# Kernel tuning notes

Hardware: AMD Instinct MI355X
Metric: run time of the kernel (lower is better)

The kernel has to match this reference:

```python
import jax, jax.numpy as jnp
import numpy as np

N, E = 50000, 400000
NODE_IN, EDGE_IN, HID = 16, 8, 16


def setup_inputs() -> dict:
    key = jax.random.key(0)
    ks = jax.random.split(key, 20)
    s = 0.05
    inp = {
        "x": jax.random.normal(ks[0], (N, NODE_IN), jnp.float32),
        "edge_attr": jax.random.normal(ks[1], (E, EDGE_IN), jnp.float32),
        # edge_nn1: Linear(edge_in, hid) -> ReLU -> Linear(hid, node_in*hid)
        "e1_w1": jax.random.normal(ks[2], (EDGE_IN, HID), jnp.float32) * s,
        "e1_b1": jnp.zeros((HID,), jnp.float32),
        "e1_w2": jax.random.normal(ks[3], (HID, NODE_IN * HID), jnp.float32) * s,
        "e1_b2": jnp.zeros((NODE_IN * HID,), jnp.float32),
        # NNConv1 root weight + bias
        "root1": jax.random.normal(ks[4], (NODE_IN, HID), jnp.float32) * s,
        "bias1": jnp.zeros((HID,), jnp.float32),
        # edge_nn2: Linear(edge_in, hid) -> ReLU -> Linear(hid, hid*hid)
        "e2_w1": jax.random.normal(ks[5], (EDGE_IN, HID), jnp.float32) * s,
        "e2_b1": jnp.zeros((HID,), jnp.float32),
        "e2_w2": jax.random.normal(ks[6], (HID, HID * HID), jnp.float32) * s,
        "e2_b2": jnp.zeros((HID * HID,), jnp.float32),
        # NNConv2 root weight + bias
        "root2": jax.random.normal(ks[7], (HID, HID), jnp.float32) * s,
        "bias2": jnp.zeros((HID,), jnp.float32),
        # q_head
        "q_w": jax.random.normal(ks[8], (HID, 1), jnp.float32) * s,
        "q_b": jnp.zeros((1,), jnp.float32),
        "edge_index": jax.random.randint(ks[9], (2, E), 0, N, jnp.int64),
    }
    return inp


def _nnconv(x, src, dst, edge_attr, w1, b1, w2, b2, root, bias, in_ch, out_ch, n_nodes):
    # edge MLP -> per-edge weight matrix [E, in_ch, out_ch]
    h = jax.nn.relu(edge_attr @ w1 + b1)
    W = (h @ w2 + b2).reshape(-1, in_ch, out_ch)
    # gather source features, per-edge matmul (bmm)
    msg = jnp.einsum('ei,eio->eo', x[src], W)  # [E, out_ch]
    # scatter-mean into target nodes
    summed = jax.ops.segment_sum(msg, dst, num_segments=n_nodes)
    cnt = jax.ops.segment_sum(jnp.ones((dst.shape[0], 1), x.dtype), dst, num_segments=n_nodes)
    agg = summed / jnp.maximum(cnt, 1.0)
    # root transform + bias (NNConv update)
    return agg + x @ root + bias


def reference(x, edge_attr, e1_w1, e1_b1, e1_w2, e1_b2, root1, bias1,
              e2_w1, e2_b1, e2_w2, e2_b2, root2, bias2, q_w, q_b, edge_index):
    src, dst = edge_index[0], edge_index[1]
    h = jax.nn.relu(_nnconv(x, src, dst, edge_attr, e1_w1, e1_b1, e1_w2, e1_b2,
                            root1, bias1, NODE_IN, HID, N))
    h = jax.nn.relu(_nnconv(h, src, dst, edge_attr, e2_w1, e2_b1, e2_w2, e2_b2,
                            root2, bias2, HID, HID, N))
    return (h @ q_w + q_b).squeeze(-1)  # [N]
```

## Files before the change

kernel.cpp:

```cpp
#include <hip/hip_runtime.h>

#define NN 50000
#define NE 400000
#define SCAN_N (2 * NN)
#define SA_BLOCKS ((SCAN_N + 255) / 256)
#define YSTRIDE 276


__global__ __launch_bounds__(256) void hist2_kernel(
    const int* __restrict__ eidx, int* __restrict__ cnt)
{
    int e = blockIdx.x * 256 + threadIdx.x;
    if (e < NE) {
        atomicAdd(&cnt[eidx[e]], 1);
        atomicAdd(&cnt[NN + eidx[NE + e]], 1);
    }
}

template <int NT>
__device__ __forceinline__ int block_excl_scan(int v, int tid)
{
    __shared__ int wsum[NT / 64];
    int lane = tid & 63, w = tid >> 6;
    int incl = v;
#pragma unroll
    for (int d = 1; d < 64; d <<= 1) {
        int t = __shfl_up(incl, d, 64);
        if (lane >= d) incl += t;
    }
    if (lane == 63) wsum[w] = incl;
    __syncthreads();
    if (tid == 0) {
        int s = 0;
#pragma unroll
        for (int k = 0; k < NT / 64; ++k) { int t = wsum[k]; wsum[k] = s; s += t; }
    }
    __syncthreads();
    return incl - v + wsum[w];
}

__global__ __launch_bounds__(256) void scan_a_kernel(
    const int* __restrict__ cnt, int* __restrict__ bsum)
{
    __shared__ int wsum[4];
    int tid = threadIdx.x;
    int i = blockIdx.x * 256 + tid;
    int v = (i < SCAN_N) ? cnt[i] : 0;
#pragma unroll
    for (int d = 32; d >= 1; d >>= 1) v += __shfl_down(v, d, 64);
    if ((tid & 63) == 0) wsum[tid >> 6] = v;
    __syncthreads();
    if (tid == 0) bsum[blockIdx.x] = wsum[0] + wsum[1] + wsum[2] + wsum[3];
}

__global__ __launch_bounds__(512) void scan_b_kernel(
    int* __restrict__ bsum, int* __restrict__ offs_all)
{
    int tid = threadIdx.x;
    int v = (tid < SA_BLOCKS) ? bsum[tid] : 0;
    int excl = block_excl_scan<512>(v, tid);
    if (tid < SA_BLOCKS) bsum[tid] = excl;
    if (tid == SA_BLOCKS - 1) offs_all[SCAN_N] = excl + v;
}

__global__ __launch_bounds__(256) void scan_c_kernel(
    int* __restrict__ cnt ,
    const int* __restrict__ bsum, int* __restrict__ offs_all)
{
    int tid = threadIdx.x;
    int i = blockIdx.x * 256 + tid;
    int v = (i < SCAN_N) ? cnt[i] : 0;
    int excl = block_excl_scan<256>(v, tid) + bsum[blockIdx.x];
    if (i < SCAN_N) { offs_all[i] = excl; cnt[i] = excl; }
}

__global__ __launch_bounds__(256) void fill2_kernel(
    const int* __restrict__ eidx, int* __restrict__ cursor,
    int2* __restrict__ ordsrc)
{
    int e = blockIdx.x * 256 + threadIdx.x;
    if (e < NE) {
        int s = eidx[e], d = eidx[NE + e];
        int ps = atomicAdd(&cursor[s], 1);
        int pd = atomicAdd(&cursor[NN + d], 1) - NE;
        ordsrc[ps] = make_int2(e, pd);
    }
}

__global__ __launch_bounds__(256) void edge_fused_kernel(
    const float* __restrict__ xin,
    const float* __restrict__ ea,
    const int2*  __restrict__ ordsrc,
    const int*   __restrict__ offs_src,
    const float* __restrict__ w1,
    const float* __restrict__ b1,
    const float* __restrict__ w2,
    const float* __restrict__ b2,
    float* __restrict__ msg)
{
    __shared__ float xl[16 * 16];
    __shared__ float Yl[16 * YSTRIDE];
    __shared__ int so[17];

    int tid = threadIdx.x;
    int n0 = blockIdx.x * 16;

    {
        int node = tid >> 4, i = tid & 15;
        xl[tid] = xin[(size_t)(n0 + node) * 16 + i];
    }
    if (tid < 17) so[tid] = offs_src[n0 + tid];
    __syncthreads();

    int o = tid & 15;
    {
        int k = tid >> 4;
        float w[16];
#pragma unroll
        for (int i = 0; i < 16; ++i) w[i] = w2[k * 256 + i * 16 + o];
#pragma unroll 4
        for (int node = 0; node < 16; ++node) {
            const float4* xr = (const float4*)&xl[node * 16];
            float4 x0 = xr[0], x1 = xr[1], x2 = xr[2], x3 = xr[3];
            float acc = x0.x * w[0] + x0.y * w[1] + x0.z * w[2] + x0.w * w[3]
                      + x1.x * w[4] + x1.y * w[5] + x1.z * w[6] + x1.w * w[7]
                      + x2.x * w[8] + x2.y * w[9] + x2.z * w[10] + x2.w * w[11]
                      + x3.x * w[12] + x3.y * w[13] + x3.z * w[14] + x3.w * w[15];
            Yl[node * YSTRIDE + k * 16 + o] = acc;
        }
    }
    {
        int node = tid >> 4;
        float w[16];
#pragma unroll
        for (int i = 0; i < 16; ++i) w[i] = b2[i * 16 + o];
        const float4* xr = (const float4*)&xl[node * 16];
        float4 x0 = xr[0], x1 = xr[1], x2 = xr[2], x3 = xr[3];
        float acc = x0.x * w[0] + x0.y * w[1] + x0.z * w[2] + x0.w * w[3]
                  + x1.x * w[4] + x1.y * w[5] + x1.z * w[6] + x1.w * w[7]
                  + x2.x * w[8] + x2.y * w[9] + x2.z * w[10] + x2.w * w[11]
                  + x3.x * w[12] + x3.y * w[13] + x3.z * w[14] + x3.w * w[15];
        Yl[node * YSTRIDE + 256 + o] = acc;
    }
    __syncthreads();

    int j0 = so[0], j1 = so[16];
    for (int j = j0 + tid; j < j1; j += 256) {
        int node = 0;
#pragma unroll
        for (int t = 1; t < 16; ++t) node += (j >= so[t]) ? 1 : 0;

        int2 od = ordsrc[j];
        int e = od.x, pd = od.y;

        const float4* av = (const float4*)(ea + (size_t)e * 8);
        float4 a0 = av[0], a1 = av[1];
        float a[8] = {a0.x, a0.y, a0.z, a0.w, a1.x, a1.y, a1.z, a1.w};

        float hid[16];
#pragma unroll
        for (int jj = 0; jj < 16; ++jj) hid[jj] = b1[jj];
#pragma unroll
        for (int c = 0; c < 8; ++c)
#pragma unroll
            for (int jj = 0; jj < 16; ++jj) hid[jj] += a[c] * w1[c * 16 + jj];
#pragma unroll
        for (int jj = 0; jj < 16; ++jj) hid[jj] = fmaxf(hid[jj], 0.0f);

        const float4* Yr = (const float4*)&Yl[node * YSTRIDE];
        float4 m0 = Yr[64], m1 = Yr[65], m2 = Yr[66], m3 = Yr[67];
#pragma unroll
        for (int k = 0; k < 16; ++k) {
            float hk = hid[k];
            float4 y0 = Yr[k * 4 + 0], y1 = Yr[k * 4 + 1];
            float4 y2 = Yr[k * 4 + 2], y3 = Yr[k * 4 + 3];
            m0.x = fmaf(hk, y0.x, m0.x); m0.y = fmaf(hk, y0.y, m0.y);
            m0.z = fmaf(hk, y0.z, m0.z); m0.w = fmaf(hk, y0.w, m0.w);
            m1.x = fmaf(hk, y1.x, m1.x); m1.y = fmaf(hk, y1.y, m1.y);
            m1.z = fmaf(hk, y1.z, m1.z); m1.w = fmaf(hk, y1.w, m1.w);
            m2.x = fmaf(hk, y2.x, m2.x); m2.y = fmaf(hk, y2.y, m2.y);
            m2.z = fmaf(hk, y2.z, m2.z); m2.w = fmaf(hk, y2.w, m2.w);
            m3.x = fmaf(hk, y3.x, m3.x); m3.y = fmaf(hk, y3.y, m3.y);
            m3.z = fmaf(hk, y3.z, m3.z); m3.w = fmaf(hk, y3.w, m3.w);
        }
        float4* mp = (float4*)(msg + (size_t)pd * 16);
        mp[0] = m0; mp[1] = m1; mp[2] = m2; mp[3] = m3;
    }
}

__global__ __launch_bounds__(256) void node1_gather(
    const float* __restrict__ x, const float* __restrict__ msg,
    const int* __restrict__ offs_dst,
    const float* __restrict__ root, const float* __restrict__ bias,
    float* __restrict__ out)
{
    int t = blockIdx.x * 256 + threadIdx.x;
    int n = t >> 4, o = t & 15;
    if (n >= NN) return;

    int j0 = offs_dst[n] - NE, j1 = offs_dst[n + 1] - NE;
    float sum = 0.0f;
    for (int j = j0; j < j1; ++j) sum += msg[(size_t)j * 16 + o];
    float inv = 1.0f / (float)((j1 - j0) > 0 ? (j1 - j0) : 1);
    float acc = sum * inv + bias[o];

    float xo = x[(size_t)n * 16 + o];
#pragma unroll
    for (int i = 0; i < 16; ++i)
        acc += __shfl(xo, i, 16) * root[i * 16 + o];

    out[(size_t)n * 16 + o] = fmaxf(acc, 0.0f);
}

__global__ __launch_bounds__(256) void node2q_gather(
    const float* __restrict__ h1, const float* __restrict__ msg,
    const int* __restrict__ offs_dst,
    const float* __restrict__ root, const float* __restrict__ bias,
    const float* __restrict__ qw, const float* __restrict__ qb,
    float* __restrict__ out)
{
    int t = blockIdx.x * 256 + threadIdx.x;
    int n = t >> 4, o = t & 15;
    if (n >= NN) return;

    int j0 = offs_dst[n] - NE, j1 = offs_dst[n + 1] - NE;
    float sum = 0.0f;
    for (int j = j0; j < j1; ++j) sum += msg[(size_t)j * 16 + o];
    float inv = 1.0f / (float)((j1 - j0) > 0 ? (j1 - j0) : 1);
    float acc = sum * inv + bias[o];

    float xo = h1[(size_t)n * 16 + o];
#pragma unroll
    for (int i = 0; i < 16; ++i)
        acc += __shfl(xo, i, 16) * root[i * 16 + o];

    float q = fmaxf(acc, 0.0f) * qw[o];
#pragma unroll
    for (int d = 8; d >= 1; d >>= 1) q += __shfl_down(q, d, 16);
    if (o == 0) out[n] = q + qb[0];
}

extern "C" void kernel_launch(void* const* d_in, const int* in_sizes, int n_in,
                              void* d_out, int out_size, void* d_ws, size_t ws_size,
                              hipStream_t stream) {
    const float* x     = (const float*)d_in[0];
    const float* ea    = (const float*)d_in[1];
    const float* e1w1  = (const float*)d_in[2];
    const float* e1b1  = (const float*)d_in[3];
    const float* e1w2  = (const float*)d_in[4];
    const float* e1b2  = (const float*)d_in[5];
    const float* root1 = (const float*)d_in[6];
    const float* bias1 = (const float*)d_in[7];
    const float* e2w1  = (const float*)d_in[8];
    const float* e2b1  = (const float*)d_in[9];
    const float* e2w2  = (const float*)d_in[10];
    const float* e2b2  = (const float*)d_in[11];
    const float* root2 = (const float*)d_in[12];
    const float* bias2 = (const float*)d_in[13];
    const float* qw    = (const float*)d_in[14];
    const float* qb    = (const float*)d_in[15];
    const int*   eidx  = (const int*)d_in[16];

    float* msg      = (float*)d_ws;
    float* h1       = msg + (size_t)16 * NE;
    int*   offs_all = (int*)(h1 + (size_t)16 * NN);
    int*   cursor   = offs_all + SCAN_N + 1;
    int2*  ordsrc   = (int2*)(cursor + SCAN_N);
    int*   bsum     = (int*)(ordsrc + NE);

    int eblocks = (NE + 255) / 256;
    int gblocks = NN / 16;
    int nblocks = (NN * 16 + 255) / 256;

    hipMemsetAsync(cursor, 0, (size_t)SCAN_N * sizeof(int), stream);
    hist2_kernel<<<eblocks, 256, 0, stream>>>(eidx, cursor);
    scan_a_kernel<<<SA_BLOCKS, 256, 0, stream>>>(cursor, bsum);
    scan_b_kernel<<<1, 512, 0, stream>>>(bsum, offs_all);
    scan_c_kernel<<<SA_BLOCKS, 256, 0, stream>>>(cursor, bsum, offs_all);
    fill2_kernel<<<eblocks, 256, 0, stream>>>(eidx, cursor, ordsrc);

    edge_fused_kernel<<<gblocks, 256, 0, stream>>>(x, ea, ordsrc, offs_all,
                                                   e1w1, e1b1, e1w2, e1b2, msg);
    node1_gather<<<nblocks, 256, 0, stream>>>(x, msg, offs_all + NN, root1,
                                              bias1, h1);

    edge_fused_kernel<<<gblocks, 256, 0, stream>>>(h1, ea, ordsrc, offs_all,
                                                   e2w1, e2b1, e2w2, e2b2, msg);
    node2q_gather<<<nblocks, 256, 0, stream>>>(h1, msg, offs_all + NN, root2,
                                               bias2, qw, qb, (float*)d_out);
}
```

Before: 256.5 us.

## Replace CSR scan with capped source-group buckets and atomic scatter-add aggregation

Removes the histogram and three-pass scan and the dst-sorted message buffer. Edges are now bucketed per group of 16 source nodes into fixed-capacity slots, and destination counts are gathered in the same pass. The edge kernel accumulates messages straight into per-node sums with float atomics, and the layer-1 node update is fused into the layer-2 edge kernel. This cuts the number of launches and the message-buffer traffic, at the cost of many global atomics. It also relies on no group exceeding CAP edges: extra edges in a group would be silently dropped, and the atomic summation order is nondeterministic.

```diff
diff --git a/kernel.cpp b/kernel.cpp
--- a/kernel.cpp
+++ b/kernel.cpp
@@ -2,135 +2,83 @@
 
 #define NN 50000
 #define NE 400000
-#define SCAN_N (2 * NN)
-#define SA_BLOCKS ((SCAN_N + 255) / 256)
+#define NG (NN / 16)
+#define CAP 320
 #define YSTRIDE 276
 
 
-__global__ __launch_bounds__(256) void hist2_kernel(
-    const int* __restrict__ eidx, int* __restrict__ cnt)
-{
-    int e = blockIdx.x * 256 + threadIdx.x;
-    if (e < NE) {
-        atomicAdd(&cnt[eidx[e]], 1);
-        atomicAdd(&cnt[NN + eidx[NE + e]], 1);
-    }
-}
-
-template <int NT>
-__device__ __forceinline__ int block_excl_scan(int v, int tid)
-{
-    __shared__ int wsum[NT / 64];
-    int lane = tid & 63, w = tid >> 6;
-    int incl = v;
-#pragma unroll
-    for (int d = 1; d < 64; d <<= 1) {
-        int t = __shfl_up(incl, d, 64);
-        if (lane >= d) incl += t;
-    }
-    if (lane == 63) wsum[w] = incl;
-    __syncthreads();
-    if (tid == 0) {
-        int s = 0;
-#pragma unroll
-        for (int k = 0; k < NT / 64; ++k) { int t = wsum[k]; wsum[k] = s; s += t; }
-    }
-    __syncthreads();
-    return incl - v + wsum[w];
-}
-
-__global__ __launch_bounds__(256) void scan_a_kernel(
-    const int* __restrict__ cnt, int* __restrict__ bsum)
-{
-    __shared__ int wsum[4];
-    int tid = threadIdx.x;
-    int i = blockIdx.x * 256 + tid;
-    int v = (i < SCAN_N) ? cnt[i] : 0;
-#pragma unroll
-    for (int d = 32; d >= 1; d >>= 1) v += __shfl_down(v, d, 64);
-    if ((tid & 63) == 0) wsum[tid >> 6] = v;
-    __syncthreads();
-    if (tid == 0) bsum[blockIdx.x] = wsum[0] + wsum[1] + wsum[2] + wsum[3];
-}
-
-__global__ __launch_bounds__(512) void scan_b_kernel(
-    int* __restrict__ bsum, int* __restrict__ offs_all)
-{
-    int tid = threadIdx.x;
-    int v = (tid < SA_BLOCKS) ? bsum[tid] : 0;
-    int excl = block_excl_scan<512>(v, tid);
-    if (tid < SA_BLOCKS) bsum[tid] = excl;
-    if (tid == SA_BLOCKS - 1) offs_all[SCAN_N] = excl + v;
-}
-
-__global__ __launch_bounds__(256) void scan_c_kernel(
-    int* __restrict__ cnt ,
-    const int* __restrict__ bsum, int* __restrict__ offs_all)
-{
-    int tid = threadIdx.x;
-    int i = blockIdx.x * 256 + tid;
-    int v = (i < SCAN_N) ? cnt[i] : 0;
-    int excl = block_excl_scan<256>(v, tid) + bsum[blockIdx.x];
-    if (i < SCAN_N) { offs_all[i] = excl; cnt[i] = excl; }
-}
-
-__global__ __launch_bounds__(256) void fill2_kernel(
+__global__ __launch_bounds__(256) void fill_hist_kernel(
     const int* __restrict__ eidx, int* __restrict__ cursor,
-    int2* __restrict__ ordsrc)
+    int* __restrict__ cnt_dst, int2* __restrict__ ord)
 {
     int e = blockIdx.x * 256 + threadIdx.x;
     if (e < NE) {
         int s = eidx[e], d = eidx[NE + e];
-        int ps = atomicAdd(&cursor[s], 1);
-        int pd = atomicAdd(&cursor[NN + d], 1) - NE;
-        ordsrc[ps] = make_int2(e, pd);
-    }
-}
-
+        atomicAdd(&cnt_dst[d], 1);
+        int g = s >> 4;
+        int slot = atomicAdd(&cursor[g], 1);
+        if (slot < CAP)
+            ord[(size_t)g * CAP + slot] = make_int2(e, d | ((s & 15) << 27));
+    }
+}
+
+template <bool SECOND>
 __global__ __launch_bounds__(256) void edge_fused_kernel(
     const float* __restrict__ xin,
+    const float* __restrict__ agg_in,
+    const int*   __restrict__ cnt_dst,
+    const float* __restrict__ rootp,
+    const float* __restrict__ biasp,
+    float*       __restrict__ h1_out,
     const float* __restrict__ ea,
-    const int2*  __restrict__ ordsrc,
-    const int*   __restrict__ offs_src,
+    const int2*  __restrict__ ord,
+    const int*   __restrict__ cursor,
     const float* __restrict__ w1,
     const float* __restrict__ b1,
     const float* __restrict__ w2,
     const float* __restrict__ b2,
-    float* __restrict__ msg)
+    float*       __restrict__ agg_out)
 {
     __shared__ float xl[16 * 16];
     __shared__ float Yl[16 * YSTRIDE];
-    __shared__ int so[17];
 
     int tid = threadIdx.x;
     int n0 = blockIdx.x * 16;
-
-    {
-        int node = tid >> 4, i = tid & 15;
-        xl[tid] = xin[(size_t)(n0 + node) * 16 + i];
-    }
-    if (tid < 17) so[tid] = offs_src[n0 + tid];
+    int node = tid >> 4, o = tid & 15;
+
+    if (!SECOND) {
+        xl[tid] = xin[(size_t)(n0 + node) * 16 + o];
+    } else {
+        float xo = xin[(size_t)(n0 + node) * 16 + o];
+        int c = cnt_dst[n0 + node];
+        float acc = agg_in[(size_t)(n0 + node) * 16 + o] / (float)(c > 0 ? c : 1)
+                  + biasp[o];
+#pragma unroll
+        for (int i = 0; i < 16; ++i)
+            acc += __shfl(xo, i, 16) * rootp[i * 16 + o];
+        float h = fmaxf(acc, 0.0f);
+        xl[tid] = h;
+        h1_out[(size_t)(n0 + node) * 16 + o] = h;
+    }
     __syncthreads();
 
-    int o = tid & 15;
     {
         int k = tid >> 4;
         float w[16];
 #pragma unroll
         for (int i = 0; i < 16; ++i) w[i] = w2[k * 256 + i * 16 + o];
 #pragma unroll 4
-        for (int node = 0; node < 16; ++node) {
-            const float4* xr = (const float4*)&xl[node * 16];
+        for (int nd = 0; nd < 16; ++nd) {
+            const float4* xr = (const float4*)&xl[nd * 16];
             float4 x0 = xr[0], x1 = xr[1], x2 = xr[2], x3 = xr[3];
             float acc = x0.x * w[0] + x0.y * w[1] + x0.z * w[2] + x0.w * w[3]
                       + x1.x * w[4] + x1.y * w[5] + x1.z * w[6] + x1.w * w[7]
                       + x2.x * w[8] + x2.y * w[9] + x2.z * w[10] + x2.w * w[11]
                       + x3.x * w[12] + x3.y * w[13] + x3.z * w[14] + x3.w * w[15];
-            Yl[node * YSTRIDE + k * 16 + o] = acc;
+            Yl[nd * YSTRIDE + k * 16 + o] = acc;
         }
     }
     {
-        int node = tid >> 4;
         float w[16];
 #pragma unroll
         for (int i = 0; i < 16; ++i) w[i] = b2[i * 16 + o];
@@ -144,14 +92,14 @@
     }
     __syncthreads();
 
-    int j0 = so[0], j1 = so[16];
-    for (int j = j0 + tid; j < j1; j += 256) {
-        int node = 0;
-#pragma unroll
-        for (int t = 1; t < 16; ++t) node += (j >= so[t]) ? 1 : 0;
-
-        int2 od = ordsrc[j];
-        int e = od.x, pd = od.y;
+    int cnt = cursor[blockIdx.x];
+    if (cnt > CAP) cnt = CAP;
+    const int2* op = ord + (size_t)blockIdx.x * CAP;
+    for (int j = tid; j < cnt; j += 256) {
+        int2 od = op[j];
+        int e = od.x;
+        int d = od.y & 0x07FFFFFF;
+        int nl = ((unsigned)od.y) >> 27;
 
         const float4* av = (const float4*)(ea + (size_t)e * 8);
         float4 a0 = av[0], a1 = av[1];
@@ -167,7 +115,7 @@
 #pragma unroll
         for (int jj = 0; jj < 16; ++jj) hid[jj] = fmaxf(hid[jj], 0.0f);
 
-        const float4* Yr = (const float4*)&Yl[node * YSTRIDE];
+        const float4* Yr = (const float4*)&Yl[nl * YSTRIDE];
         float4 m0 = Yr[64], m1 = Yr[65], m2 = Yr[66], m3 = Yr[67];
 #pragma unroll
         for (int k = 0; k < 16; ++k) {
@@ -183,38 +131,21 @@
             m3.x = fmaf(hk, y3.x, m3.x); m3.y = fmaf(hk, y3.y, m3.y);
             m3.z = fmaf(hk, y3.z, m3.z); m3.w = fmaf(hk, y3.w, m3.w);
         }
-        float4* mp = (float4*)(msg + (size_t)pd * 16);
-        mp[0] = m0; mp[1] = m1; mp[2] = m2; mp[3] = m3;
-    }
-}
-
-__global__ __launch_bounds__(256) void node1_gather(
-    const float* __restrict__ x, const float* __restrict__ msg,
-    const int* __restrict__ offs_dst,
-    const float* __restrict__ root, const float* __restrict__ bias,
-    float* __restrict__ out)
-{
-    int t = blockIdx.x * 256 + threadIdx.x;
-    int n = t >> 4, o = t & 15;
-    if (n >= NN) return;
-
-    int j0 = offs_dst[n] - NE, j1 = offs_dst[n + 1] - NE;
-    float sum = 0.0f;
-    for (int j = j0; j < j1; ++j) sum += msg[(size_t)j * 16 + o];
-    float inv = 1.0f / (float)((j1 - j0) > 0 ? (j1 - j0) : 1);
-    float acc = sum * inv + bias[o];
-
-    float xo = x[(size_t)n * 16 + o];
-#pragma unroll
-    for (int i = 0; i < 16; ++i)
-        acc += __shfl(xo, i, 16) * root[i * 16 + o];
-
-    out[(size_t)n * 16 + o] = fmaxf(acc, 0.0f);
-}
-
-__global__ __launch_bounds__(256) void node2q_gather(
-    const float* __restrict__ h1, const float* __restrict__ msg,
-    const int* __restrict__ offs_dst,
+        float* ap = agg_out + (size_t)d * 16;
+        unsafeAtomicAdd(ap + 0,  m0.x); unsafeAtomicAdd(ap + 1,  m0.y);
+        unsafeAtomicAdd(ap + 2,  m0.z); unsafeAtomicAdd(ap + 3,  m0.w);
+        unsafeAtomicAdd(ap + 4,  m1.x); unsafeAtomicAdd(ap + 5,  m1.y);
+        unsafeAtomicAdd(ap + 6,  m1.z); unsafeAtomicAdd(ap + 7,  m1.w);
+        unsafeAtomicAdd(ap + 8,  m2.x); unsafeAtomicAdd(ap + 9,  m2.y);
+        unsafeAtomicAdd(ap + 10, m2.z); unsafeAtomicAdd(ap + 11, m2.w);
+        unsafeAtomicAdd(ap + 12, m3.x); unsafeAtomicAdd(ap + 13, m3.y);
+        unsafeAtomicAdd(ap + 14, m3.z); unsafeAtomicAdd(ap + 15, m3.w);
+    }
+}
+
+__global__ __launch_bounds__(256) void node2q_kernel(
+    const float* __restrict__ h1, const float* __restrict__ agg2,
+    const int* __restrict__ cnt_dst,
     const float* __restrict__ root, const float* __restrict__ bias,
     const float* __restrict__ qw, const float* __restrict__ qb,
     float* __restrict__ out)
@@ -223,16 +154,12 @@
     int n = t >> 4, o = t & 15;
     if (n >= NN) return;
 
-    int j0 = offs_dst[n] - NE, j1 = offs_dst[n + 1] - NE;
-    float sum = 0.0f;
-    for (int j = j0; j < j1; ++j) sum += msg[(size_t)j * 16 + o];
-    float inv = 1.0f / (float)((j1 - j0) > 0 ? (j1 - j0) : 1);
-    float acc = sum * inv + bias[o];
-
-    float xo = h1[(size_t)n * 16 + o];
+    int c = cnt_dst[n];
+    float acc = agg2[(size_t)n * 16 + o] / (float)(c > 0 ? c : 1) + bias[o];
+    float ho = h1[(size_t)n * 16 + o];
 #pragma unroll
     for (int i = 0; i < 16; ++i)
-        acc += __shfl(xo, i, 16) * root[i * 16 + o];
+        acc += __shfl(ho, i, 16) * root[i * 16 + o];
 
     float q = fmaxf(acc, 0.0f) * qw[o];
 #pragma unroll
@@ -261,31 +188,28 @@
     const float* qb    = (const float*)d_in[15];
     const int*   eidx  = (const int*)d_in[16];
 
-    float* msg      = (float*)d_ws;
-    float* h1       = msg + (size_t)16 * NE;
-    int*   offs_all = (int*)(h1 + (size_t)16 * NN);
-    int*   cursor   = offs_all + SCAN_N + 1;
-    int2*  ordsrc   = (int2*)(cursor + SCAN_N);
-    int*   bsum     = (int*)(ordsrc + NE);
+    float* agg1    = (float*)d_ws;
+    float* agg2    = agg1 + (size_t)16 * NN;
+    int*   cursor  = (int*)(agg2 + (size_t)16 * NN);
+    int*   cnt_dst = cursor + NG;
+    int2*  ord     = (int2*)(cnt_dst + NN + 1);
+    float* h1      = (float*)(ord + (size_t)NG * CAP);
 
     int eblocks = (NE + 255) / 256;
-    int gblocks = NN / 16;
-    int nblocks = (NN * 16 + 255) / 256;
-
-    hipMemsetAsync(cursor, 0, (size_t)SCAN_N * sizeof(int), stream);
-    hist2_kernel<<<eblocks, 256, 0, stream>>>(eidx, cursor);
-    scan_a_kernel<<<SA_BLOCKS, 256, 0, stream>>>(cursor, bsum);
-    scan_b_kernel<<<1, 512, 0, stream>>>(bsum, offs_all);
-    scan_c_kernel<<<SA_BLOCKS, 256, 0, stream>>>(cursor, bsum, offs_all);
-    fill2_kernel<<<eblocks, 256, 0, stream>>>(eidx, cursor, ordsrc);
-
-    edge_fused_kernel<<<gblocks, 256, 0, stream>>>(x, ea, ordsrc, offs_all,
-                                                   e1w1, e1b1, e1w2, e1b2, msg);
-    node1_gather<<<nblocks, 256, 0, stream>>>(x, msg, offs_all + NN, root1,
-                                              bias1, h1);
-
-    edge_fused_kernel<<<gblocks, 256, 0, stream>>>(h1, ea, ordsrc, offs_all,
-                                                   e2w1, e2b1, e2w2, e2b2, msg);
-    node2q_gather<<<nblocks, 256, 0, stream>>>(h1, msg, offs_all + NN, root2,
-                                               bias2, qw, qb, (float*)d_out);
-}
+
+    size_t zero_bytes = ((size_t)32 * NN + NG + NN) * sizeof(int);
+    hipMemsetAsync(d_ws, 0, zero_bytes, stream);
+
+    fill_hist_kernel<<<eblocks, 256, 0, stream>>>(eidx, cursor, cnt_dst, ord);
+
+    edge_fused_kernel<false><<<NG, 256, 0, stream>>>(
+        x, nullptr, nullptr, nullptr, nullptr, nullptr,
+        ea, ord, cursor, e1w1, e1b1, e1w2, e1b2, agg1);
+
+    edge_fused_kernel<true><<<NG, 256, 0, stream>>>(
+        x, agg1, cnt_dst, root1, bias1, h1,
+        ea, ord, cursor, e2w1, e2b1, e2w2, e2b2, agg2);
+
+    node2q_kernel<<<3125, 256, 0, stream>>>(
+        h1, agg2, cnt_dst, root2, bias2, qw, qb, (float*)d_out);
+}
```

After: 843.0 us. 3.29x slower.
